# Kernel tuning notes

Hardware: AMD Instinct MI355X
Metric: run time of the kernel (lower is better)

Reference implementation:

```python
import jax, jax.numpy as jnp
import numpy as np

NUM_SEGMENTS = 64  # label ids in [0, 64); id 0 = background/excluded
ALPHA, BETA, GAMMA = 1.0, 1.0, 0.001
DELTA_V, DELTA_D = 0.0, 1.5


def setup_inputs() -> dict:
    key = jax.random.key(0)
    k1, k2, k3 = jax.random.split(key, 3)
    embd = jax.random.normal(k1, (1, 16, 32, 512, 512), dtype=jnp.float32)
    trgt = jax.random.randint(k2, (1, 1, 32, 512, 512), 0, NUM_SEGMENTS, dtype=jnp.int32)
    mask = jax.random.randint(k3, (1, 1, 32, 512, 512), 0, 2, dtype=jnp.int32)
    return {"embd": embd, "trgt": trgt, "mask": mask}


def _mean_loss(embd, trgt, mask):
    C = embd.shape[1]
    # masked labels: background (0) absorbs masked-out voxels
    seg = (trgt * (mask > 0).astype(trgt.dtype)).reshape(-1)            # [P]
    x = embd[0].reshape(C, -1).T                                        # [P, C]

    # fused scatter-mean (segment reduce) replacing the per-id python loop
    counts = jax.ops.segment_sum(jnp.ones(seg.shape, x.dtype), seg,
                                 num_segments=NUM_SEGMENTS)             # [L]
    sums = jax.ops.segment_sum(x, seg, num_segments=NUM_SEGMENTS)       # [L, C]
    safe = jnp.maximum(counts, 1.0)
    means = sums / safe[:, None]                                        # [L, C]

    present = (counts > 0).at[0].set(False)                             # id 0 excluded
    K = jnp.sum(present).astype(x.dtype)

    # internal term: per-voxel L1 distance to own-object mean, hinge, squared,
    # mean per object, then averaged over objects
    margin = jnp.sum(jnp.abs(x - means[seg]), axis=-1) - DELTA_V        # [P]
    per_pix = jnp.maximum(margin, 0.0) ** 2
    per_id = jax.ops.segment_sum(per_pix, seg, num_segments=NUM_SEGMENTS) / safe
    loss_int = jnp.sum(jnp.where(present, per_id, 0.0)) / jnp.maximum(1.0, K)

    # external term: pairwise L1 margin between object means (all off-diag pairs)
    dist = jnp.sum(jnp.abs(means[:, None, :] - means[None, :, :]), axis=-1)  # [L, L]
    eye = jnp.eye(NUM_SEGMENTS, dtype=bool)
    pair = present[:, None] & present[None, :] & (~eye)
    m_ext = jnp.maximum(2.0 * DELTA_D - dist, 0.0) ** 2
    loss_ext = jnp.sum(jnp.where(pair, m_ext, 0.0)) / jnp.maximum(1.0, K * (K - 1.0))

    # regularization: mean L1 norm of object means
    nrm = jnp.sum(jnp.abs(means), axis=-1)                              # [L]
    loss_nrm = jnp.sum(jnp.where(present, nrm, 0.0)) / jnp.maximum(1.0, K)

    return ALPHA * loss_int + BETA * loss_ext + GAMMA * loss_nrm


def reference(embd, trgt, mask):
    return _mean_loss(embd, trgt, mask)
```

## Files before the change

kernel.cpp:

```cpp
#include <hip/hip_runtime.h>
#include <cstdint>
#include <cstddef>

#define NSEG 64
#define NCH 16
#define ALPHA 1.0f
#define BETA 1.0f
#define GAMMA 0.001f
#define DELTA_D 1.5f


__global__ __launch_bounds__(256) void init_kernel(float* __restrict__ ws) {
    int i = blockIdx.x * 256 + threadIdx.x;
    if (i < 4096) ws[i] = 0.f;
}

__global__ __launch_bounds__(256) void pass1_kernel(
    const float* __restrict__ embd, const int* __restrict__ trgt,
    const int* __restrict__ mask, float* __restrict__ gsums,
    unsigned int* __restrict__ gcounts, unsigned char* __restrict__ segs,
    int P)
{
    __shared__ float lsums[NCH * NSEG];
    __shared__ unsigned int lcounts[NSEG];
    for (int i = threadIdx.x; i < NCH * NSEG; i += 256) lsums[i] = 0.f;
    if (threadIdx.x < NSEG) lcounts[threadIdx.x] = 0u;
    __syncthreads();

    const int P4 = P >> 2;
    const size_t stride = (size_t)gridDim.x * 256;
    const float4* __restrict__ embd4 = (const float4*)embd;
    const int4* __restrict__ trgt4 = (const int4*)trgt;
    const int4* __restrict__ mask4 = (const int4*)mask;

    for (size_t p4 = (size_t)blockIdx.x * 256 + threadIdx.x; p4 < (size_t)P4; p4 += stride) {
        int4 t = trgt4[p4];
        int4 m = mask4[p4];
        int s0 = (m.x > 0) ? t.x : 0;
        int s1 = (m.y > 0) ? t.y : 0;
        int s2 = (m.z > 0) ? t.z : 0;
        int s3 = (m.w > 0) ? t.w : 0;
        if (segs) {
            uchar4 pk;
            pk.x = (unsigned char)s0; pk.y = (unsigned char)s1;
            pk.z = (unsigned char)s2; pk.w = (unsigned char)s3;
            ((uchar4*)segs)[p4] = pk;
        }
        if (s0) atomicAdd(&lcounts[s0], 1u);
        if (s1) atomicAdd(&lcounts[s1], 1u);
        if (s2) atomicAdd(&lcounts[s2], 1u);
        if (s3) atomicAdd(&lcounts[s3], 1u);
        if ((s0 | s1 | s2 | s3) != 0) {
            #pragma unroll
            for (int c = 0; c < NCH; ++c) {
                float4 v = embd4[(size_t)c * P4 + p4];
                if (s0) atomicAdd(&lsums[c * NSEG + s0], v.x);
                if (s1) atomicAdd(&lsums[c * NSEG + s1], v.y);
                if (s2) atomicAdd(&lsums[c * NSEG + s2], v.z);
                if (s3) atomicAdd(&lsums[c * NSEG + s3], v.w);
            }
        }
    }
    for (size_t p = (size_t)(P4 << 2) + blockIdx.x * 256 + threadIdx.x; p < (size_t)P; p += stride) {
        int s = (mask[p] > 0) ? trgt[p] : 0;
        if (segs) segs[p] = (unsigned char)s;
        if (s) {
            atomicAdd(&lcounts[s], 1u);
            #pragma unroll
            for (int c = 0; c < NCH; ++c)
                atomicAdd(&lsums[c * NSEG + s], embd[(size_t)c * P + p]);
        }
    }
    __syncthreads();
    for (int i = threadIdx.x; i < NCH * NSEG; i += 256) {
        float v = lsums[i];
        if (v != 0.f) atomicAdd(&gsums[i], v);
    }
    if (threadIdx.x < NSEG) {
        unsigned int v = lcounts[threadIdx.x];
        if (v) atomicAdd(&gcounts[threadIdx.x], v);
    }
}

__global__ __launch_bounds__(256) void mid_kernel(
    const float* __restrict__ gsums, const unsigned int* __restrict__ gcounts,
    float* __restrict__ gmeans, float* __restrict__ scalars)
{
    __shared__ float smeans[NCH * NSEG];
    __shared__ float scnt[NSEG];
    __shared__ float s_ext, s_nrm;
    int tid = threadIdx.x;
    if (tid == 0) { s_ext = 0.f; s_nrm = 0.f; }
    if (tid < NSEG) scnt[tid] = (float)gcounts[tid];
    __syncthreads();
    for (int i = tid; i < NCH * NSEG; i += 256) {
        int l = i & (NSEG - 1);
        float mean = gsums[i] / fmaxf(scnt[l], 1.f);
        smeans[i] = mean;
        gmeans[i] = mean;
    }
    __syncthreads();
    if (tid < NSEG) {
        int l = tid;
        if (l != 0 && scnt[l] > 0.f) {
            float a = 0.f;
            #pragma unroll
            for (int c = 0; c < NCH; ++c) a += fabsf(smeans[c * NSEG + l]);
            atomicAdd(&s_nrm, a);
        }
    }
    float eacc = 0.f;
    for (int q = tid; q < NSEG * NSEG; q += 256) {
        int l1 = q >> 6, l2 = q & 63;
        if (l1 != l2 && l1 != 0 && l2 != 0 && scnt[l1] > 0.f && scnt[l2] > 0.f) {
            float d = 0.f;
            #pragma unroll
            for (int c = 0; c < NCH; ++c)
                d += fabsf(smeans[c * NSEG + l1] - smeans[c * NSEG + l2]);
            float mm = fmaxf(2.f * DELTA_D - d, 0.f);
            eacc += mm * mm;
        }
    }
    if (eacc != 0.f) atomicAdd(&s_ext, eacc);
    __syncthreads();
    if (tid == 0) {
        float K = 0.f;
        for (int l = 1; l < NSEG; ++l) if (scnt[l] > 0.f) K += 1.f;
        scalars[0] = K;
        scalars[1] = BETA * s_ext / fmaxf(1.f, K * (K - 1.f))
                   + GAMMA * s_nrm / fmaxf(1.f, K);
    }
}

__global__ __launch_bounds__(256) void pass2_kernel(
    const float* __restrict__ embd, const unsigned char* __restrict__ segs,
    const int* __restrict__ trgt, const int* __restrict__ mask,
    const float* __restrict__ gmeans, float* __restrict__ gper, int P)
{
    __shared__ float lmeans[NCH * NSEG];
    __shared__ float lper[NSEG];
    for (int i = threadIdx.x; i < NCH * NSEG; i += 256) lmeans[i] = gmeans[i];
    if (threadIdx.x < NSEG) lper[threadIdx.x] = 0.f;
    __syncthreads();

    const int P4 = P >> 2;
    const size_t stride = (size_t)gridDim.x * 256;
    const float4* __restrict__ embd4 = (const float4*)embd;

    for (size_t p4 = (size_t)blockIdx.x * 256 + threadIdx.x; p4 < (size_t)P4; p4 += stride) {
        int s0, s1, s2, s3;
        if (segs) {
            uchar4 pk = ((const uchar4*)segs)[p4];
            s0 = pk.x; s1 = pk.y; s2 = pk.z; s3 = pk.w;
        } else {
            int4 t = ((const int4*)trgt)[p4];
            int4 m = ((const int4*)mask)[p4];
            s0 = (m.x > 0) ? t.x : 0;
            s1 = (m.y > 0) ? t.y : 0;
            s2 = (m.z > 0) ? t.z : 0;
            s3 = (m.w > 0) ? t.w : 0;
        }
        if ((s0 | s1 | s2 | s3) != 0) {
            float a0 = 0.f, a1 = 0.f, a2 = 0.f, a3 = 0.f;
            #pragma unroll
            for (int c = 0; c < NCH; ++c) {
                float4 v = embd4[(size_t)c * P4 + p4];
                const float* mrow = &lmeans[c * NSEG];
                a0 += fabsf(v.x - mrow[s0]);
                a1 += fabsf(v.y - mrow[s1]);
                a2 += fabsf(v.z - mrow[s2]);
                a3 += fabsf(v.w - mrow[s3]);
            }
            if (s0) { float h = fmaxf(a0, 0.f); atomicAdd(&lper[s0], h * h); }
            if (s1) { float h = fmaxf(a1, 0.f); atomicAdd(&lper[s1], h * h); }
            if (s2) { float h = fmaxf(a2, 0.f); atomicAdd(&lper[s2], h * h); }
            if (s3) { float h = fmaxf(a3, 0.f); atomicAdd(&lper[s3], h * h); }
        }
    }
    for (size_t p = (size_t)(P4 << 2) + blockIdx.x * 256 + threadIdx.x; p < (size_t)P; p += stride) {
        int s = segs ? (int)segs[p] : ((mask[p] > 0) ? trgt[p] : 0);
        if (s) {
            float a = 0.f;
            #pragma unroll
            for (int c = 0; c < NCH; ++c)
                a += fabsf(embd[(size_t)c * P + p] - lmeans[c * NSEG + s]);
            float h = fmaxf(a, 0.f);
            atomicAdd(&lper[s], h * h);
        }
    }
    __syncthreads();
    if (threadIdx.x < NSEG) {
        float v = lper[threadIdx.x];
        if (v != 0.f) atomicAdd(&gper[threadIdx.x], v);
    }
}

__global__ __launch_bounds__(64) void final_kernel(
    const float* __restrict__ gper, const unsigned int* __restrict__ gcounts,
    const float* __restrict__ scalars, float* __restrict__ out)
{
    int l = threadIdx.x;
    float cnt = (float)gcounts[l];
    bool present = (l != 0) && (cnt > 0.f);
    float v = present ? gper[l] / fmaxf(cnt, 1.f) : 0.f;
    #pragma unroll
    for (int off = 32; off > 0; off >>= 1) v += __shfl_down(v, off);
    if (l == 0) {
        float K = scalars[0];
        float loss_int = v / fmaxf(1.f, K);
        out[0] = ALPHA * loss_int + scalars[1];
    }
}

extern "C" void kernel_launch(void* const* d_in, const int* in_sizes, int n_in,
                              void* d_out, int out_size, void* d_ws, size_t ws_size,
                              hipStream_t stream) {
    const float* embd = (const float*)d_in[0];
    const int* trgt = (const int*)d_in[1];
    const int* mask = (const int*)d_in[2];
    const int P = in_sizes[1];

    float* ws = (float*)d_ws;
    float* gsums = ws;
    unsigned int* gcounts = (unsigned int*)(ws + 1024);
    float* gper = ws + 1088;
    float* gmeans = ws + 1152;
    float* scalars = ws + 2176;

    unsigned char* segs = nullptr;
    const size_t seg_off = 16384;
    if (ws_size >= seg_off + (size_t)P) segs = (unsigned char*)d_ws + seg_off;

    init_kernel<<<16, 256, 0, stream>>>(ws);
    pass1_kernel<<<1024, 256, 0, stream>>>(embd, trgt, mask, gsums, gcounts, segs, P);
    mid_kernel<<<1, 256, 0, stream>>>(gsums, gcounts, gmeans, scalars);
    pass2_kernel<<<1024, 256, 0, stream>>>(embd, segs, trgt, mask, gmeans, gper, P);
    final_kernel<<<1, 64, 0, stream>>>(gper, gcounts, scalars, (float*)d_out);
}
```

Measured before the change: 1.009 ms.

## Split segment-id computation into its own kernel and batch channel loads

Moves label masking, uint8 segment packing and counting into a separate seg_kernel, so pass1 reads the compact segs buffer instead of trgt and mask. Both passes now load all 16 float4 channel values into registers before doing any atomics or distance math, which gives more memory-level parallelism. The cost is an extra kernel launch, an extra read of trgt and mask plus a write of segs that pass1 then rereads, and higher register pressure from the 64-float staging array.

After: 1.050 ms. +4.1%, slower.

```diff
diff --git a/kernel.cpp b/kernel.cpp
--- a/kernel.cpp
+++ b/kernel.cpp
@@ -15,21 +15,16 @@
     if (i < 4096) ws[i] = 0.f;
 }
 
-__global__ __launch_bounds__(256) void pass1_kernel(
-    const float* __restrict__ embd, const int* __restrict__ trgt,
-    const int* __restrict__ mask, float* __restrict__ gsums,
-    unsigned int* __restrict__ gcounts, unsigned char* __restrict__ segs,
-    int P)
-{
-    __shared__ float lsums[NCH * NSEG];
+__global__ __launch_bounds__(256) void seg_kernel(
+    const int* __restrict__ trgt, const int* __restrict__ mask,
+    unsigned char* __restrict__ segs, unsigned int* __restrict__ gcounts, int P)
+{
     __shared__ unsigned int lcounts[NSEG];
-    for (int i = threadIdx.x; i < NCH * NSEG; i += 256) lsums[i] = 0.f;
     if (threadIdx.x < NSEG) lcounts[threadIdx.x] = 0u;
     __syncthreads();
 
     const int P4 = P >> 2;
     const size_t stride = (size_t)gridDim.x * 256;
-    const float4* __restrict__ embd4 = (const float4*)embd;
     const int4* __restrict__ trgt4 = (const int4*)trgt;
     const int4* __restrict__ mask4 = (const int4*)mask;
 
@@ -50,97 +45,26 @@
         if (s1) atomicAdd(&lcounts[s1], 1u);
         if (s2) atomicAdd(&lcounts[s2], 1u);
         if (s3) atomicAdd(&lcounts[s3], 1u);
-        if ((s0 | s1 | s2 | s3) != 0) {
-            #pragma unroll
-            for (int c = 0; c < NCH; ++c) {
-                float4 v = embd4[(size_t)c * P4 + p4];
-                if (s0) atomicAdd(&lsums[c * NSEG + s0], v.x);
-                if (s1) atomicAdd(&lsums[c * NSEG + s1], v.y);
-                if (s2) atomicAdd(&lsums[c * NSEG + s2], v.z);
-                if (s3) atomicAdd(&lsums[c * NSEG + s3], v.w);
-            }
-        }
     }
     for (size_t p = (size_t)(P4 << 2) + blockIdx.x * 256 + threadIdx.x; p < (size_t)P; p += stride) {
         int s = (mask[p] > 0) ? trgt[p] : 0;
         if (segs) segs[p] = (unsigned char)s;
-        if (s) {
-            atomicAdd(&lcounts[s], 1u);
-            #pragma unroll
-            for (int c = 0; c < NCH; ++c)
-                atomicAdd(&lsums[c * NSEG + s], embd[(size_t)c * P + p]);
-        }
-    }
-    __syncthreads();
-    for (int i = threadIdx.x; i < NCH * NSEG; i += 256) {
-        float v = lsums[i];
-        if (v != 0.f) atomicAdd(&gsums[i], v);
-    }
+        if (s) atomicAdd(&lcounts[s], 1u);
+    }
+    __syncthreads();
     if (threadIdx.x < NSEG) {
         unsigned int v = lcounts[threadIdx.x];
         if (v) atomicAdd(&gcounts[threadIdx.x], v);
     }
 }
 
-__global__ __launch_bounds__(256) void mid_kernel(
-    const float* __restrict__ gsums, const unsigned int* __restrict__ gcounts,
-    float* __restrict__ gmeans, float* __restrict__ scalars)
-{
-    __shared__ float smeans[NCH * NSEG];
-    __shared__ float scnt[NSEG];
-    __shared__ float s_ext, s_nrm;
-    int tid = threadIdx.x;
-    if (tid == 0) { s_ext = 0.f; s_nrm = 0.f; }
-    if (tid < NSEG) scnt[tid] = (float)gcounts[tid];
-    __syncthreads();
-    for (int i = tid; i < NCH * NSEG; i += 256) {
-        int l = i & (NSEG - 1);
-        float mean = gsums[i] / fmaxf(scnt[l], 1.f);
-        smeans[i] = mean;
-        gmeans[i] = mean;
-    }
-    __syncthreads();
-    if (tid < NSEG) {
-        int l = tid;
-        if (l != 0 && scnt[l] > 0.f) {
-            float a = 0.f;
-            #pragma unroll
-            for (int c = 0; c < NCH; ++c) a += fabsf(smeans[c * NSEG + l]);
-            atomicAdd(&s_nrm, a);
-        }
-    }
-    float eacc = 0.f;
-    for (int q = tid; q < NSEG * NSEG; q += 256) {
-        int l1 = q >> 6, l2 = q & 63;
-        if (l1 != l2 && l1 != 0 && l2 != 0 && scnt[l1] > 0.f && scnt[l2] > 0.f) {
-            float d = 0.f;
-            #pragma unroll
-            for (int c = 0; c < NCH; ++c)
-                d += fabsf(smeans[c * NSEG + l1] - smeans[c * NSEG + l2]);
-            float mm = fmaxf(2.f * DELTA_D - d, 0.f);
-            eacc += mm * mm;
-        }
-    }
-    if (eacc != 0.f) atomicAdd(&s_ext, eacc);
-    __syncthreads();
-    if (tid == 0) {
-        float K = 0.f;
-        for (int l = 1; l < NSEG; ++l) if (scnt[l] > 0.f) K += 1.f;
-        scalars[0] = K;
-        scalars[1] = BETA * s_ext / fmaxf(1.f, K * (K - 1.f))
-                   + GAMMA * s_nrm / fmaxf(1.f, K);
-    }
-}
-
-__global__ __launch_bounds__(256) void pass2_kernel(
+__global__ __launch_bounds__(256) void pass1_kernel(
     const float* __restrict__ embd, const unsigned char* __restrict__ segs,
     const int* __restrict__ trgt, const int* __restrict__ mask,
-    const float* __restrict__ gmeans, float* __restrict__ gper, int P)
-{
-    __shared__ float lmeans[NCH * NSEG];
-    __shared__ float lper[NSEG];
-    for (int i = threadIdx.x; i < NCH * NSEG; i += 256) lmeans[i] = gmeans[i];
-    if (threadIdx.x < NSEG) lper[threadIdx.x] = 0.f;
+    float* __restrict__ gsums, int P)
+{
+    __shared__ float lsums[NCH * NSEG];
+    for (int i = threadIdx.x; i < NCH * NSEG; i += 256) lsums[i] = 0.f;
     __syncthreads();
 
     const int P4 = P >> 2;
@@ -160,22 +84,132 @@
             s2 = (m.z > 0) ? t.z : 0;
             s3 = (m.w > 0) ? t.w : 0;
         }
-        if ((s0 | s1 | s2 | s3) != 0) {
-            float a0 = 0.f, a1 = 0.f, a2 = 0.f, a3 = 0.f;
-            #pragma unroll
-            for (int c = 0; c < NCH; ++c) {
-                float4 v = embd4[(size_t)c * P4 + p4];
-                const float* mrow = &lmeans[c * NSEG];
-                a0 += fabsf(v.x - mrow[s0]);
-                a1 += fabsf(v.y - mrow[s1]);
-                a2 += fabsf(v.z - mrow[s2]);
-                a3 += fabsf(v.w - mrow[s3]);
-            }
-            if (s0) { float h = fmaxf(a0, 0.f); atomicAdd(&lper[s0], h * h); }
-            if (s1) { float h = fmaxf(a1, 0.f); atomicAdd(&lper[s1], h * h); }
-            if (s2) { float h = fmaxf(a2, 0.f); atomicAdd(&lper[s2], h * h); }
-            if (s3) { float h = fmaxf(a3, 0.f); atomicAdd(&lper[s3], h * h); }
-        }
+        if ((s0 | s1 | s2 | s3) == 0) continue;
+
+        float4 v[NCH];
+        #pragma unroll
+        for (int c = 0; c < NCH; ++c) v[c] = embd4[(size_t)c * P4 + p4];
+
+        #pragma unroll
+        for (int c = 0; c < NCH; ++c) {
+            if (s0) atomicAdd(&lsums[c * NSEG + s0], v[c].x);
+            if (s1) atomicAdd(&lsums[c * NSEG + s1], v[c].y);
+            if (s2) atomicAdd(&lsums[c * NSEG + s2], v[c].z);
+            if (s3) atomicAdd(&lsums[c * NSEG + s3], v[c].w);
+        }
+    }
+    for (size_t p = (size_t)(P4 << 2) + blockIdx.x * 256 + threadIdx.x; p < (size_t)P; p += stride) {
+        int s = segs ? (int)segs[p] : ((mask[p] > 0) ? trgt[p] : 0);
+        if (s) {
+            #pragma unroll
+            for (int c = 0; c < NCH; ++c)
+                atomicAdd(&lsums[c * NSEG + s], embd[(size_t)c * P + p]);
+        }
+    }
+    __syncthreads();
+    for (int i = threadIdx.x; i < NCH * NSEG; i += 256) {
+        float v = lsums[i];
+        if (v != 0.f) atomicAdd(&gsums[i], v);
+    }
+}
+
+__global__ __launch_bounds__(256) void mid_kernel(
+    const float* __restrict__ gsums, const unsigned int* __restrict__ gcounts,
+    float* __restrict__ gmeans, float* __restrict__ scalars)
+{
+    __shared__ float smeans[NCH * NSEG];
+    __shared__ float scnt[NSEG];
+    __shared__ float s_ext, s_nrm;
+    int tid = threadIdx.x;
+    if (tid == 0) { s_ext = 0.f; s_nrm = 0.f; }
+    if (tid < NSEG) scnt[tid] = (float)gcounts[tid];
+    __syncthreads();
+    for (int i = tid; i < NCH * NSEG; i += 256) {
+        int l = i & (NSEG - 1);
+        float mean = gsums[i] / fmaxf(scnt[l], 1.f);
+        smeans[i] = mean;
+        gmeans[i] = mean;
+    }
+    __syncthreads();
+    if (tid < NSEG) {
+        int l = tid;
+        if (l != 0 && scnt[l] > 0.f) {
+            float a = 0.f;
+            #pragma unroll
+            for (int c = 0; c < NCH; ++c) a += fabsf(smeans[c * NSEG + l]);
+            atomicAdd(&s_nrm, a);
+        }
+    }
+    float eacc = 0.f;
+    for (int q = tid; q < NSEG * NSEG; q += 256) {
+        int l1 = q >> 6, l2 = q & 63;
+        if (l1 != l2 && l1 != 0 && l2 != 0 && scnt[l1] > 0.f && scnt[l2] > 0.f) {
+            float d = 0.f;
+            #pragma unroll
+            for (int c = 0; c < NCH; ++c)
+                d += fabsf(smeans[c * NSEG + l1] - smeans[c * NSEG + l2]);
+            float mm = fmaxf(2.f * DELTA_D - d, 0.f);
+            eacc += mm * mm;
+        }
+    }
+    if (eacc != 0.f) atomicAdd(&s_ext, eacc);
+    __syncthreads();
+    if (tid == 0) {
+        float K = 0.f;
+        for (int l = 1; l < NSEG; ++l) if (scnt[l] > 0.f) K += 1.f;
+        scalars[0] = K;
+        scalars[1] = BETA * s_ext / fmaxf(1.f, K * (K - 1.f))
+                   + GAMMA * s_nrm / fmaxf(1.f, K);
+    }
+}
+
+__global__ __launch_bounds__(256) void pass2_kernel(
+    const float* __restrict__ embd, const unsigned char* __restrict__ segs,
+    const int* __restrict__ trgt, const int* __restrict__ mask,
+    const float* __restrict__ gmeans, float* __restrict__ gper, int P)
+{
+    __shared__ float lmeans[NCH * NSEG];
+    __shared__ float lper[NSEG];
+    for (int i = threadIdx.x; i < NCH * NSEG; i += 256) lmeans[i] = gmeans[i];
+    if (threadIdx.x < NSEG) lper[threadIdx.x] = 0.f;
+    __syncthreads();
+
+    const int P4 = P >> 2;
+    const size_t stride = (size_t)gridDim.x * 256;
+    const float4* __restrict__ embd4 = (const float4*)embd;
+
+    for (size_t p4 = (size_t)blockIdx.x * 256 + threadIdx.x; p4 < (size_t)P4; p4 += stride) {
+        int s0, s1, s2, s3;
+        if (segs) {
+            uchar4 pk = ((const uchar4*)segs)[p4];
+            s0 = pk.x; s1 = pk.y; s2 = pk.z; s3 = pk.w;
+        } else {
+            int4 t = ((const int4*)trgt)[p4];
+            int4 m = ((const int4*)mask)[p4];
+            s0 = (m.x > 0) ? t.x : 0;
+            s1 = (m.y > 0) ? t.y : 0;
+            s2 = (m.z > 0) ? t.z : 0;
+            s3 = (m.w > 0) ? t.w : 0;
+        }
+        if ((s0 | s1 | s2 | s3) == 0) continue;
+
+        float4 v[NCH];
+        #pragma unroll
+        for (int c = 0; c < NCH; ++c) v[c] = embd4[(size_t)c * P4 + p4];
+
+        float a0 = 0.f, a1 = 0.f, a2 = 0.f, a3 = 0.f;
+        #pragma unroll
+        for (int c = 0; c < NCH; ++c) {
+            const float* mrow = &lmeans[c * NSEG];
+            a0 += fabsf(v[c].x - mrow[s0]);
+            a1 += fabsf(v[c].y - mrow[s1]);
+            a2 += fabsf(v[c].z - mrow[s2]);
+            a3 += fabsf(v[c].w - mrow[s3]);
+        }
+        if (s0) { float h = fmaxf(a0, 0.f); atomicAdd(&lper[s0], h * h); }
+        if (s1) { float h = fmaxf(a1, 0.f); atomicAdd(&lper[s1], h * h); }
+        if (s2) { float h = fmaxf(a2, 0.f); atomicAdd(&lper[s2], h * h); }
+        if (s3) { float h = fmaxf(a3, 0.f); atomicAdd(&lper[s3], h * h); }
     }
     for (size_t p = (size_t)(P4 << 2) + blockIdx.x * 256 + threadIdx.x; p < (size_t)P; p += stride) {
         int s = segs ? (int)segs[p] : ((mask[p] > 0) ? trgt[p] : 0);
@@ -232,7 +266,8 @@
     if (ws_size >= seg_off + (size_t)P) segs = (unsigned char*)d_ws + seg_off;
 
     init_kernel<<<16, 256, 0, stream>>>(ws);
-    pass1_kernel<<<1024, 256, 0, stream>>>(embd, trgt, mask, gsums, gcounts, segs, P);
+    seg_kernel<<<1024, 256, 0, stream>>>(trgt, mask, segs, gcounts, P);
+    pass1_kernel<<<1024, 256, 0, stream>>>(embd, segs, trgt, mask, gsums, P);
     mid_kernel<<<1, 256, 0, stream>>>(gsums, gcounts, gmeans, scalars);
     pass2_kernel<<<1024, 256, 0, stream>>>(embd, segs, trgt, mask, gmeans, gper, P);
     final_kernel<<<1, 64, 0, stream>>>(gper, gcounts, scalars, (float*)d_out);
```

## Replace grid-stride loops with one-shot blocks processing four quads per thread

Applied to the files above, without the earlier changes.

Both passes switch from a fixed 1024-block grid-stride loop to a grid sized so each thread handles exactly KQ=4 float4 quads, with no loop. Per channel the four embedding loads are issued together before the shared-memory atomics or abs-diff accumulation, which raises memory-level parallelism. The per-pixel "skip if all background" branch is removed, so embeddings are loaded even for quads that are all zero. The grid becomes very large (about 2048 blocks), and each of those blocks pays its own shared-memory init and global flush of 1024 sums.

Result: slower. 1.051 ms (+4.2%).

```diff
diff --git a/kernel.cpp b/kernel.cpp
--- a/kernel.cpp
+++ b/kernel.cpp
@@ -9,6 +9,10 @@
 #define GAMMA 0.001f
 #define DELTA_D 1.5f
 
+#define TPB 256
+#define KQ 4
+#define WQ (TPB * KQ)
+
 
 __global__ __launch_bounds__(256) void init_kernel(float* __restrict__ ws) {
     int i = blockIdx.x * 256 + threadIdx.x;
@@ -17,62 +21,93 @@
 
 __global__ __launch_bounds__(256) void pass1_kernel(
     const float* __restrict__ embd, const int* __restrict__ trgt,
-    const int* __restrict__ mask, float* __restrict__ gsums,
-    unsigned int* __restrict__ gcounts, unsigned char* __restrict__ segs,
-    int P)
+    const int* __restrict__ mask, unsigned char* __restrict__ segs,
+    float* __restrict__ gsums, unsigned int* __restrict__ gcounts, int P)
 {
     __shared__ float lsums[NCH * NSEG];
     __shared__ unsigned int lcounts[NSEG];
-    for (int i = threadIdx.x; i < NCH * NSEG; i += 256) lsums[i] = 0.f;
+    for (int i = threadIdx.x; i < NCH * NSEG; i += TPB) lsums[i] = 0.f;
     if (threadIdx.x < NSEG) lcounts[threadIdx.x] = 0u;
     __syncthreads();
 
     const int P4 = P >> 2;
-    const size_t stride = (size_t)gridDim.x * 256;
-    const float4* __restrict__ embd4 = (const float4*)embd;
-    const int4* __restrict__ trgt4 = (const int4*)trgt;
-    const int4* __restrict__ mask4 = (const int4*)mask;
-
-    for (size_t p4 = (size_t)blockIdx.x * 256 + threadIdx.x; p4 < (size_t)P4; p4 += stride) {
-        int4 t = trgt4[p4];
-        int4 m = mask4[p4];
-        int s0 = (m.x > 0) ? t.x : 0;
-        int s1 = (m.y > 0) ? t.y : 0;
-        int s2 = (m.z > 0) ? t.z : 0;
-        int s3 = (m.w > 0) ? t.w : 0;
-        if (segs) {
-            uchar4 pk;
-            pk.x = (unsigned char)s0; pk.y = (unsigned char)s1;
-            pk.z = (unsigned char)s2; pk.w = (unsigned char)s3;
-            ((uchar4*)segs)[p4] = pk;
-        }
-        if (s0) atomicAdd(&lcounts[s0], 1u);
-        if (s1) atomicAdd(&lcounts[s1], 1u);
-        if (s2) atomicAdd(&lcounts[s2], 1u);
-        if (s3) atomicAdd(&lcounts[s3], 1u);
-        if ((s0 | s1 | s2 | s3) != 0) {
-            #pragma unroll
-            for (int c = 0; c < NCH; ++c) {
-                float4 v = embd4[(size_t)c * P4 + p4];
-                if (s0) atomicAdd(&lsums[c * NSEG + s0], v.x);
-                if (s1) atomicAdd(&lsums[c * NSEG + s1], v.y);
-                if (s2) atomicAdd(&lsums[c * NSEG + s2], v.z);
-                if (s3) atomicAdd(&lsums[c * NSEG + s3], v.w);
+    const int t = threadIdx.x;
+
+    if (P4 > 0) {
+        const size_t base = (size_t)blockIdx.x * WQ;
+        const int4* __restrict__ trgt4 = (const int4*)trgt;
+        const int4* __restrict__ mask4 = (const int4*)mask;
+        const float4* __restrict__ embd4 = (const float4*)embd;
+
+        size_t q[KQ];
+        bool val[KQ];
+        unsigned int pk[KQ];
+
+        #pragma unroll
+        for (int k = 0; k < KQ; ++k) {
+            size_t qq = base + (size_t)k * TPB + t;
+            val[k] = qq < (size_t)P4;
+            if (!val[k]) qq = (size_t)P4 - 1;
+            q[k] = qq;
+        }
+
+        #pragma unroll
+        for (int k = 0; k < KQ; ++k) {
+            int4 tt = trgt4[q[k]];
+            int4 mm = mask4[q[k]];
+            int s0 = (mm.x > 0) ? tt.x : 0;
+            int s1 = (mm.y > 0) ? tt.y : 0;
+            int s2 = (mm.z > 0) ? tt.z : 0;
+            int s3 = (mm.w > 0) ? tt.w : 0;
+            if (!val[k]) { s0 = s1 = s2 = s3 = 0; }
+            pk[k] = (unsigned)s0 | ((unsigned)s1 << 8) |
+                    ((unsigned)s2 << 16) | ((unsigned)s3 << 24);
+            if (val[k] && segs) {
+                uchar4 u;
+                u.x = (unsigned char)s0; u.y = (unsigned char)s1;
+                u.z = (unsigned char)s2; u.w = (unsigned char)s3;
+                ((uchar4*)segs)[q[k]] = u;
             }
-        }
-    }
-    for (size_t p = (size_t)(P4 << 2) + blockIdx.x * 256 + threadIdx.x; p < (size_t)P; p += stride) {
+            if (s0) atomicAdd(&lcounts[s0], 1u);
+            if (s1) atomicAdd(&lcounts[s1], 1u);
+            if (s2) atomicAdd(&lcounts[s2], 1u);
+            if (s3) atomicAdd(&lcounts[s3], 1u);
+        }
+
+        #pragma unroll 2
+        for (int c = 0; c < NCH; ++c) {
+            float4 v[KQ];
+            #pragma unroll
+            for (int k = 0; k < KQ; ++k)
+                v[k] = embd4[(size_t)c * P4 + q[k]];
+            float* __restrict__ row = &lsums[c * NSEG];
+            #pragma unroll
+            for (int k = 0; k < KQ; ++k) {
+                int s0 = pk[k] & 255;
+                int s1 = (pk[k] >> 8) & 255;
+                int s2 = (pk[k] >> 16) & 255;
+                int s3 = pk[k] >> 24;
+                if (s0) atomicAdd(&row[s0], v[k].x);
+                if (s1) atomicAdd(&row[s1], v[k].y);
+                if (s2) atomicAdd(&row[s2], v[k].z);
+                if (s3) atomicAdd(&row[s3], v[k].w);
+            }
+        }
+    }
+
+    for (size_t p = (size_t)P4 * 4 + (size_t)blockIdx.x * TPB + t;
+         p < (size_t)P; p += (size_t)gridDim.x * TPB) {
         int s = (mask[p] > 0) ? trgt[p] : 0;
         if (segs) segs[p] = (unsigned char)s;
         if (s) {
             atomicAdd(&lcounts[s], 1u);
-            #pragma unroll
             for (int c = 0; c < NCH; ++c)
                 atomicAdd(&lsums[c * NSEG + s], embd[(size_t)c * P + p]);
         }
     }
-    __syncthreads();
-    for (int i = threadIdx.x; i < NCH * NSEG; i += 256) {
+
+    __syncthreads();
+    for (int i = threadIdx.x; i < NCH * NSEG; i += TPB) {
         float v = lsums[i];
         if (v != 0.f) atomicAdd(&gsums[i], v);
     }
@@ -139,55 +174,99 @@
 {
     __shared__ float lmeans[NCH * NSEG];
     __shared__ float lper[NSEG];
-    for (int i = threadIdx.x; i < NCH * NSEG; i += 256) lmeans[i] = gmeans[i];
+    for (int i = threadIdx.x; i < NCH * NSEG; i += TPB) lmeans[i] = gmeans[i];
     if (threadIdx.x < NSEG) lper[threadIdx.x] = 0.f;
     __syncthreads();
 
     const int P4 = P >> 2;
-    const size_t stride = (size_t)gridDim.x * 256;
-    const float4* __restrict__ embd4 = (const float4*)embd;
-
-    for (size_t p4 = (size_t)blockIdx.x * 256 + threadIdx.x; p4 < (size_t)P4; p4 += stride) {
-        int s0, s1, s2, s3;
-        if (segs) {
-            uchar4 pk = ((const uchar4*)segs)[p4];
-            s0 = pk.x; s1 = pk.y; s2 = pk.z; s3 = pk.w;
-        } else {
-            int4 t = ((const int4*)trgt)[p4];
-            int4 m = ((const int4*)mask)[p4];
-            s0 = (m.x > 0) ? t.x : 0;
-            s1 = (m.y > 0) ? t.y : 0;
-            s2 = (m.z > 0) ? t.z : 0;
-            s3 = (m.w > 0) ? t.w : 0;
-        }
-        if ((s0 | s1 | s2 | s3) != 0) {
-            float a0 = 0.f, a1 = 0.f, a2 = 0.f, a3 = 0.f;
-            #pragma unroll
-            for (int c = 0; c < NCH; ++c) {
-                float4 v = embd4[(size_t)c * P4 + p4];
-                const float* mrow = &lmeans[c * NSEG];
-                a0 += fabsf(v.x - mrow[s0]);
-                a1 += fabsf(v.y - mrow[s1]);
-                a2 += fabsf(v.z - mrow[s2]);
-                a3 += fabsf(v.w - mrow[s3]);
+    const int t = threadIdx.x;
+
+    if (P4 > 0) {
+        const size_t base = (size_t)blockIdx.x * WQ;
+        const float4* __restrict__ embd4 = (const float4*)embd;
+
+        size_t q[KQ];
+        bool val[KQ];
+        unsigned int pk[KQ];
+
+        #pragma unroll
+        for (int k = 0; k < KQ; ++k) {
+            size_t qq = base + (size_t)k * TPB + t;
+            val[k] = qq < (size_t)P4;
+            if (!val[k]) qq = (size_t)P4 - 1;
+            q[k] = qq;
+        }
+
+        #pragma unroll
+        for (int k = 0; k < KQ; ++k) {
+            unsigned int pp;
+            if (segs) {
+                uchar4 u = ((const uchar4*)segs)[q[k]];
+                pp = (unsigned)u.x | ((unsigned)u.y << 8) |
+                     ((unsigned)u.z << 16) | ((unsigned)u.w << 24);
+            } else {
+                int4 tt = ((const int4*)trgt)[q[k]];
+                int4 mm = ((const int4*)mask)[q[k]];
+                int s0 = (mm.x > 0) ? tt.x : 0;
+                int s1 = (mm.y > 0) ? tt.y : 0;
+                int s2 = (mm.z > 0) ? tt.z : 0;
+                int s3 = (mm.w > 0) ? tt.w : 0;
+                pp = (unsigned)s0 | ((unsigned)s1 << 8) |
+                     ((unsigned)s2 << 16) | ((unsigned)s3 << 24);
             }
-            if (s0) { float h = fmaxf(a0, 0.f); atomicAdd(&lper[s0], h * h); }
-            if (s1) { float h = fmaxf(a1, 0.f); atomicAdd(&lper[s1], h * h); }
-            if (s2) { float h = fmaxf(a2, 0.f); atomicAdd(&lper[s2], h * h); }
-            if (s3) { float h = fmaxf(a3, 0.f); atomicAdd(&lper[s3], h * h); }
-        }
-    }
-    for (size_t p = (size_t)(P4 << 2) + blockIdx.x * 256 + threadIdx.x; p < (size_t)P; p += stride) {
+            if (!val[k]) pp = 0;
+            pk[k] = pp;
+        }
+
+        float4 acc[KQ];
+        #pragma unroll
+        for (int k = 0; k < KQ; ++k) acc[k] = make_float4(0.f, 0.f, 0.f, 0.f);
+
+        #pragma unroll 2
+        for (int c = 0; c < NCH; ++c) {
+            float4 v[KQ];
+            #pragma unroll
+            for (int k = 0; k < KQ; ++k)
+                v[k] = embd4[(size_t)c * P4 + q[k]];
+            const float* __restrict__ row = &lmeans[c * NSEG];
+            #pragma unroll
+            for (int k = 0; k < KQ; ++k) {
+                int s0 = pk[k] & 255;
+                int s1 = (pk[k] >> 8) & 255;
+                int s2 = (pk[k] >> 16) & 255;
+                int s3 = pk[k] >> 24;
+                acc[k].x += fabsf(v[k].x - row[s0]);
+                acc[k].y += fabsf(v[k].y - row[s1]);
+                acc[k].z += fabsf(v[k].z - row[s2]);
+                acc[k].w += fabsf(v[k].w - row[s3]);
+            }
+        }
+
+        #pragma unroll
+        for (int k = 0; k < KQ; ++k) {
+            int s0 = pk[k] & 255;
+            int s1 = (pk[k] >> 8) & 255;
+            int s2 = (pk[k] >> 16) & 255;
+            int s3 = pk[k] >> 24;
+            if (s0) { float h = fmaxf(acc[k].x, 0.f); atomicAdd(&lper[s0], h * h); }
+            if (s1) { float h = fmaxf(acc[k].y, 0.f); atomicAdd(&lper[s1], h * h); }
+            if (s2) { float h = fmaxf(acc[k].z, 0.f); atomicAdd(&lper[s2], h * h); }
+            if (s3) { float h = fmaxf(acc[k].w, 0.f); atomicAdd(&lper[s3], h * h); }
+        }
+    }
+
+    for (size_t p = (size_t)P4 * 4 + (size_t)blockIdx.x * TPB + t;
+         p < (size_t)P; p += (size_t)gridDim.x * TPB) {
         int s = segs ? (int)segs[p] : ((mask[p] > 0) ? trgt[p] : 0);
         if (s) {
             float a = 0.f;
-            #pragma unroll
             for (int c = 0; c < NCH; ++c)
                 a += fabsf(embd[(size_t)c * P + p] - lmeans[c * NSEG + s]);
             float h = fmaxf(a, 0.f);
             atomicAdd(&lper[s], h * h);
         }
     }
+
     __syncthreads();
     if (threadIdx.x < NSEG) {
         float v = lper[threadIdx.x];
@@ -231,9 +310,12 @@
     const size_t seg_off = 16384;
     if (ws_size >= seg_off + (size_t)P) segs = (unsigned char*)d_ws + seg_off;
 
-    init_kernel<<<16, 256, 0, stream>>>(ws);
-    pass1_kernel<<<1024, 256, 0, stream>>>(embd, trgt, mask, gsums, gcounts, segs, P);
+    const int P4 = P >> 2;
+    int G = P4 > 0 ? (P4 + WQ - 1) / WQ : 1;
+
+    init_kernel<<<(4096 + 255) / 256, 256, 0, stream>>>(ws);
+    pass1_kernel<<<G, 256, 0, stream>>>(embd, trgt, mask, segs, gsums, gcounts, P);
     mid_kernel<<<1, 256, 0, stream>>>(gsums, gcounts, gmeans, scalars);
-    pass2_kernel<<<1024, 256, 0, stream>>>(embd, segs, trgt, mask, gmeans, gper, P);
+    pass2_kernel<<<G, 256, 0, stream>>>(embd, segs, trgt, mask, gmeans, gper, P);
     final_kernel<<<1, 64, 0, stream>>>(gper, gcounts, scalars, (float*)d_out);
 }
```
